# Kernel tuning notes

Measured on AMD Instinct MI355X. Metric: run time of the kernel, lower is better.

The kernel has to match this reference:

```python
import jax, jax.numpy as jnp
import numpy as np

# SLAYER neuron / simulation constants (from params)
THETA = 10.0      # spike threshold
TAU_SR = 10.0     # PSP (synaptic response) time constant
TS = 1.0          # simulation time step
TAU_RHO = 1.0     # surrogate-gradient width
SCALE_RHO = 1.0   # surrogate-gradient scale
ALPHA = float(np.exp(-TS / TAU_SR))  # leaky-filter decay per step

B, C_IN, T = 32, 156, 2048
HID, OUT = 512, 20


@jax.custom_vjp
def spike(u):
    # Hard threshold with SLAYER-style exponential surrogate gradient.
    return (u >= THETA).astype(u.dtype)

def _spike_fwd(u):
    return spike(u), u

def _spike_bwd(u, g):
    sg = (SCALE_RHO / TAU_RHO) * jnp.exp(-jnp.abs(u - THETA) / TAU_RHO)
    return (g * sg,)

spike.defvjp(_spike_fwd, _spike_bwd)


def psp(x):
    # Leaky exponential temporal filter along the LAST axis (SLAYER psp):
    # y[t] = ALPHA * y[t-1] + x[t]
    xt = jnp.moveaxis(x, -1, 0)  # [T, ...]
    def step(c, xi):
        c = ALPHA * c + xi
        return c, c
    _, y = jax.lax.scan(step, jnp.zeros_like(xt[0]), xt)
    return jnp.moveaxis(y, 0, -1)


def dense(x, W):
    # SLAYER dense layer: per-timestep fully-connected over channel dim.
    # x: [N, C, H, W, T], W: [O, C] -> [N, O, H, W, T]
    return jnp.einsum('oc,nchwt->nohwt', W, x)


def _make_perm():
    rng = np.random.default_rng(0)
    random_list = rng.permutation(np.arange(1, 40))
    perm = []
    for i in random_list:
        perm.append(2 * int(i) - 2)
        perm.append(2 * int(i) - 1)
    for i in random_list:
        perm.append(2 * int(i) - 2 + 78)
        perm.append(2 * int(i) - 1 + 78)
    return jnp.asarray(perm, dtype=jnp.int32)


def setup_inputs() -> dict:
    key = jax.random.key(0)
    k0, k1, k2, k3, k4 = jax.random.split(key, 5)
    spike_input = jax.random.randint(k0, (B, C_IN, 1, 1, T), 0, 2).astype(jnp.float32)
    W1 = jax.random.normal(k1, (HID, C_IN), dtype=jnp.float32) * (C_IN ** -0.5)
    W2 = jax.random.normal(k2, (OUT, HID), dtype=jnp.float32) * (HID ** -0.5)
    Wl1 = jax.random.normal(k3, (HID, T), dtype=jnp.float32) * (T ** -0.5)
    Wl2 = jax.random.normal(k4, (OUT, HID), dtype=jnp.float32) * (HID ** -0.5)
    perm = _make_perm()
    return {"spike_input": spike_input, "W1": W1, "W2": W2,
            "Wl1": Wl1, "Wl2": Wl2, "perm": perm}


def reference(spike_input, W1, W2, Wl1, Wl2, perm):
    # Branch 1: channel-dense over taxels, PSP + spike, twice.
    s1 = spike(psp(dense(spike_input, W1)))          # [B, HID, 1, 1, T]
    spike_output = spike(psp(dense(s1, W2)))         # [B, OUT, 1, 1, T]

    # Branch 2: transpose channel<->time, permute taxel axis, dense over time dim.
    x_t = jnp.swapaxes(spike_input, 1, 4)            # [B, T, 1, 1, C_IN]
    x_tp = x_t[..., perm]                            # gather on taxel axis
    l1 = spike(psp(dense(x_tp, Wl1)))                # [B, HID, 1, 1, C_IN]
    location_output = spike(psp(dense(l1, Wl2)))     # [B, OUT, 1, 1, C_IN]

    return jnp.concatenate([spike_output, location_output], axis=4)
```

## Files before the change

kernel.cpp:

```cpp
#include <hip/hip_runtime.h>

#define ALPHA  0.90483741803595952f
#define ALPHA8 0.44932896411722156f
#define THETA  10.0f
#define BF1    ((unsigned short)0x3F80)
#define ISCALE 0.015625f

typedef short   bf16x8 __attribute__((ext_vector_type(8)));
typedef float   f32x4  __attribute__((ext_vector_type(4)));
typedef float   f32x4v __attribute__((ext_vector_type(4)));
typedef unsigned short ushort4v __attribute__((ext_vector_type(4)));
typedef unsigned short ushort8v __attribute__((ext_vector_type(8)));
typedef unsigned char  uchar4v  __attribute__((ext_vector_type(4)));
typedef unsigned char  uchar8v  __attribute__((ext_vector_type(8)));
typedef long long i64;

__device__ __forceinline__ unsigned short f2bf(float f) {
    unsigned int x = __float_as_uint(f);
    unsigned int r = (x + 0x7FFFu + ((x >> 16) & 1u)) >> 16;
    return (unsigned short)r;
}
__device__ __forceinline__ float bf2f(unsigned short h) {
    return __uint_as_float(((unsigned int)h) << 16);
}
__device__ __forceinline__ void split2(float w, unsigned short& h0,
                                       unsigned short& h1) {
    h0 = f2bf(w);          float r0 = w - bf2f(h0);
    h1 = f2bf(r0);
}
__device__ __forceinline__ unsigned char f2fp8(float f) {
    int pk = __builtin_amdgcn_cvt_pk_fp8_f32(f, 0.f, 0, false);
    return (unsigned char)(pk & 0xFF);
}
__device__ __forceinline__ float fp82f(unsigned char b) {
    return __builtin_amdgcn_cvt_f32_fp8((int)b, 0);
}

__global__ __launch_bounds__(256) void prep_scan_pack(
    const float* __restrict__ In, unsigned char* __restrict__ Infp8,
    unsigned short* __restrict__ Pbf,
    const float* __restrict__ W1,  const float* __restrict__ W2,
    const float* __restrict__ Wl1, const float* __restrict__ Wl2,
    unsigned short* __restrict__ W1p,  unsigned char* __restrict__ W2p8,
    unsigned char* __restrict__ Wl1p8, unsigned short* __restrict__ Wl2p)
{
    const int blk = blockIdx.x;
    if (blk >= 4992) {
        const int bidx = blk - 4992;
        if (bidx >= 512 && bidx < 544) {
            int m = bidx - 512;
            for (int k = threadIdx.x; k < 512; k += 256) {
                float w = (m < 20) ? W2[(long long)m * 512 + k] : 0.f;
                unsigned char h0 = f2fp8(w);
                unsigned char h1 = f2fp8(w - fp82f(h0));
                W2p8[(long long)m * 512 + k] = h0;
                W2p8[16384 + (long long)m * 512 + k] = h1;
            }
        } else if (bidx >= 544 && bidx < 1056) {
            int m = bidx - 544;
            for (int k = threadIdx.x; k < 2048; k += 256) {
                float w = Wl1[(long long)m * 2048 + k] * 64.0f;
                unsigned char h0 = f2fp8(w);
                unsigned char h1 = f2fp8(w - fp82f(h0));
                Wl1p8[(long long)m * 2048 + k] = h0;
                Wl1p8[1048576 + (long long)m * 2048 + k] = h1;
            }
        } else {
            const float* W; unsigned short* P; int M, K, Kp, Mp, m;
            if (bidx < 512) { W = W1;  P = W1p;  M = 512; K = 156; Kp = 160; Mp = 512; m = bidx; }
            else            { W = Wl2; P = Wl2p; M = 20;  K = 512; Kp = 512; Mp = 32;  m = bidx - 1056; }
            for (int k = threadIdx.x; k < Kp; k += 256) {
                float v = (m < M && k < K) ? W[(long long)m * K + k] : 0.f;
                unsigned short h0, h1;
                split2(v, h0, h1);
                P[(long long)m * Kp + k] = h0;
                P[(long long)Mp * Kp + (long long)m * Kp + k] = h1;
            }
        }
        return;
    }

    const int row = blk;
    const int tid = threadIdx.x;
    const float* x = In + (long long)row * 2048 + tid * 8;
    const unsigned char ONE8 = f2fp8(1.0f);

    float v[8];
    *(f32x4v*)&v[0] = *(const f32x4v*)x;
    *(f32x4v*)&v[4] = *(const f32x4v*)(x + 4);

    uchar8v raw;
    #pragma unroll
    for (int k = 0; k < 8; ++k) raw[k] = (v[k] >= 0.5f) ? ONE8 : (unsigned char)0;
    *(uchar8v*)(Infp8 + (long long)row * 2048 + tid * 8) = raw;

    float y = 0.f;
    #pragma unroll
    for (int k = 0; k < 8; ++k) { y = ALPHA * y + v[k]; v[k] = y; }

    __shared__ float sc[256];
    float val = y;
    sc[tid] = val;
    float m = ALPHA8;
    for (int d = 1; d < 256; d <<= 1) {
        __syncthreads();
        float p = (tid >= d) ? sc[tid - d] : 0.f;
        __syncthreads();
        val += m * p;
        sc[tid] = val;
        m *= m;
    }
    __syncthreads();
    float carry = (tid > 0) ? sc[tid - 1] : 0.f;

    ushort8v pv;
    float ak = ALPHA;
    #pragma unroll
    for (int k = 0; k < 8; ++k) {
        float yk = v[k] + ak * carry;
        ak *= ALPHA;
        pv[k] = f2bf(yk);
    }
    *(ushort8v*)(Pbf + (long long)row * 2048 + tid * 8) = pv;
}

__global__ __launch_bounds__(256) void transposeP(
    const unsigned short* __restrict__ Pbf, unsigned short* __restrict__ PT)
{
    __shared__ unsigned short Tile[64][72];
    const int t0 = blockIdx.x * 64;
    const int c0 = blockIdx.y * 64;
    const int b  = blockIdx.z;
    const int tid = threadIdx.x;

    #pragma unroll
    for (int s = 0; s < 2; ++s) {
        int id = tid + s * 256;
        int cc = id >> 3;
        int t8 = (id & 7) * 8;
        ushort8v v = {0,0,0,0,0,0,0,0};
        if (c0 + cc < 156)
            v = *(const ushort8v*)(Pbf + (long long)(b * 156 + c0 + cc) * 2048 + t0 + t8);
        *(ushort8v*)&Tile[cc][t8] = v;
    }
    __syncthreads();

    #pragma unroll
    for (int s = 0; s < 2; ++s) {
        int id = tid + s * 256;
        int t  = id >> 3;
        int c8 = (id & 7) * 8;
        if (c0 + c8 + 7 < 160) {
            unsigned short r[8];
            #pragma unroll
            for (int j = 0; j < 8; ++j) r[j] = Tile[c8 + j][t];
            *(ushort8v*)(PT + (long long)b * 327680 + (long long)(t0 + t) * 160 + c0 + c8)
                = *(ushort8v*)r;
        }
    }
}

__global__ __launch_bounds__(256, 4) void mega_gemm1(
    const unsigned short* __restrict__ W1p,
    const unsigned short* __restrict__ PT,
    unsigned short* __restrict__ S1bits,
    const unsigned char* __restrict__ Wl1p8,
    const unsigned char* __restrict__ Infp8,
    unsigned short* __restrict__ Zp)
{
    __shared__ alignas(16) unsigned char SMEM[40960];
    const int bx  = blockIdx.x;
    const int tid = threadIdx.x;
    const int lane = tid & 63, w = tid >> 6;
    const int wy = w >> 1, wx = w & 1;
    const int l15 = lane & 15, kq = lane >> 4;

    if (bx < 4096) {
        auto As = (unsigned short (*)[2][64][40])SMEM;
        auto Bs = (unsigned short (*)[128][40])(SMEM + 20480);

        const int z  = bx >> 7;
        const int m0 = ((bx >> 4) & 7) * 64;
        const int n0 = (bx & 15) * 128;
        const unsigned short* Tb = PT + (long long)z * 327680;

        int aPl[2], aM[2], aK8[2], bT[2], bC8[2];
        #pragma unroll
        for (int s = 0; s < 2; ++s) {
            int id = tid + s * 256;
            aPl[s] = id >> 8; int rem = id & 255;
            aM[s] = rem >> 2; aK8[s] = (rem & 3) * 8;
            bT[s] = id >> 2;  bC8[s] = (id & 3) * 8;
        }

        f32x4 acc[2][4] = {};
        ushort8v aReg[2], bReg[2];

        auto loadAB = [&](int k0) {
            #pragma unroll
            for (int s = 0; s < 2; ++s)
                aReg[s] = *(const ushort8v*)(W1p + (long long)aPl[s] * 81920 +
                                             (long long)(m0 + aM[s]) * 160 + k0 + aK8[s]);
            #pragma unroll
            for (int s = 0; s < 2; ++s)
                bReg[s] = *(const ushort8v*)(Tb + (long long)(n0 + bT[s]) * 160 + k0 + bC8[s]);
        };
        auto stage = [&](int buf) {
            #pragma unroll
            for (int s = 0; s < 2; ++s) *(ushort8v*)&As[buf][aPl[s]][aM[s]][aK8[s]] = aReg[s];
            #pragma unroll
            for (int s = 0; s < 2; ++s) *(ushort8v*)&Bs[buf][bT[s]][bC8[s]] = bReg[s];
        };

        loadAB(0);
        stage(0);
        __syncthreads();

        #pragma unroll
        for (int it = 0; it < 5; ++it) {
            const int cur = it & 1;
            if (it < 4) loadAB((it + 1) * 32);

            bf16x8 bfr[4];
            #pragma unroll
            for (int nt = 0; nt < 4; ++nt)
                bfr[nt] = *(const bf16x8*)&Bs[cur][wx * 64 + nt * 16 + l15][kq * 8];
            #pragma unroll
            for (int s = 0; s < 2; ++s) {
                #pragma unroll
                for (int mt = 0; mt < 2; ++mt) {
                    bf16x8 afr = *(const bf16x8*)&As[cur][s][wy * 32 + mt * 16 + l15][kq * 8];
                    #pragma unroll
                    for (int nt = 0; nt < 4; ++nt)
                        acc[mt][nt] = __builtin_amdgcn_mfma_f32_16x16x32_bf16(
                            afr, bfr[nt], acc[mt][nt], 0, 0, 0);
                }
            }

            if (it < 4) stage(cur ^ 1);
            __syncthreads();
        }

        unsigned short* Db = S1bits + (long long)z * 512 * 128;
        #pragma unroll
        for (int mt = 0; mt < 2; ++mt) {
            #pragma unroll
            for (int i = 0; i < 4; ++i) {
                int m = m0 + wy * 32 + mt * 16 + kq * 4 + i;
                #pragma unroll
                for (int nt = 0; nt < 4; ++nt) {
                    unsigned long long mask = __ballot(acc[mt][nt][i] >= THETA);
                    if (l15 == 0) {
                        int nchunk = (n0 + wx * 64 + nt * 16) >> 4;
                        Db[(long long)m * 128 + nchunk] =
                            (unsigned short)((mask >> (kq * 16)) & 0xFFFFu);
                    }
                }
            }
        }
    } else {
        auto As8 = (unsigned char (*)[2][64][72])SMEM;
        auto Bs8 = (unsigned char (*)[128][72])(SMEM + 18432);

        const int id0 = bx - 4096;
        const int nIdx = id0 % 40;
        if (nIdx >= 39) return;
        const int rest = id0 / 40;
        const int n0  = nIdx * 128;
        const int m0  = (rest & 7) * 64;
        const int ksl = rest >> 3;
        const int ks0 = ksl * 512;

        int aPl[4], aM[4], aK8[4], bN[4], bK8[4];
        #pragma unroll
        for (int s = 0; s < 4; ++s) {
            int id = tid + s * 256;
            aPl[s] = id >> 9; int rem = id & 511;
            aM[s] = rem >> 3; aK8[s] = (rem & 7) * 8;
            bN[s] = id >> 3;  bK8[s] = (id & 7) * 8;
        }

        f32x4 acc[2][4] = {};
        uchar8v aReg[4], bReg[4];

        auto loadAB = [&](int k0) {
            #pragma unroll
            for (int s = 0; s < 4; ++s)
                aReg[s] = *(const uchar8v*)(Wl1p8 + (long long)aPl[s] * 1048576 +
                                            (long long)(m0 + aM[s]) * 2048 + k0 + aK8[s]);
            #pragma unroll
            for (int s = 0; s < 4; ++s)
                bReg[s] = *(const uchar8v*)(Infp8 + (long long)(n0 + bN[s]) * 2048 + k0 + bK8[s]);
        };
        auto stage = [&](int buf) {
            #pragma unroll
            for (int s = 0; s < 4; ++s) *(uchar8v*)&As8[buf][aPl[s]][aM[s]][aK8[s]] = aReg[s];
            #pragma unroll
            for (int s = 0; s < 4; ++s) *(uchar8v*)&Bs8[buf][bN[s]][bK8[s]] = bReg[s];
        };

        loadAB(ks0);
        stage(0);
        __syncthreads();

        for (int it = 0; it < 8; ++it) {
            const int cur = it & 1;
            if (it < 7) loadAB(ks0 + (it + 1) * 64);

            #pragma unroll
            for (int ks = 0; ks < 2; ++ks) {
                i64 bfr[4];
                #pragma unroll
                for (int nt = 0; nt < 4; ++nt)
                    bfr[nt] = *(const i64*)&Bs8[cur][wx * 64 + nt * 16 + l15][ks * 32 + kq * 8];
                #pragma unroll
                for (int s = 0; s < 2; ++s) {
                    #pragma unroll
                    for (int mt = 0; mt < 2; ++mt) {
                        i64 afr = *(const i64*)&As8[cur][s][wy * 32 + mt * 16 + l15][ks * 32 + kq * 8];
                        #pragma unroll
                        for (int nt = 0; nt < 4; ++nt)
                            acc[mt][nt] = __builtin_amdgcn_mfma_f32_16x16x32_fp8_fp8(
                                afr, bfr[nt], acc[mt][nt], 0, 0, 0);
                    }
                }
            }

            if (it < 7) stage(cur ^ 1);
            __syncthreads();
        }

        unsigned short* Tu = (unsigned short*)SMEM;
        #pragma unroll
        for (int mt = 0; mt < 2; ++mt) {
            #pragma unroll
            for (int i = 0; i < 4; ++i) {
                int mL = wy * 32 + mt * 16 + kq * 4 + i;
                #pragma unroll
                for (int nt = 0; nt < 4; ++nt) {
                    int nL = wx * 64 + nt * 16 + l15;
                    Tu[mL * 129 + nL] = f2bf(acc[mt][nt][i] * ISCALE);
                }
            }
        }
        __syncthreads();

        unsigned short* Zs = Zp + (long long)ksl * 2555904;
        #pragma unroll
        for (int s2 = 0; s2 < 32; ++s2) {
            int id = tid + s2 * 256;
            int cL = id >> 6;
            int mL = id & 63;
            int n = n0 + cL;
            int bb = n / 156, cc = n - bb * 156;
            Zs[(long long)cc * 16384 + bb * 512 + m0 + mL] = Tu[mL * 129 + cL];
        }
    }
}

__global__ __launch_bounds__(256) void mega_stage2(
    const unsigned char* __restrict__ W2p8,
    const unsigned short* __restrict__ S1bits,
    float* __restrict__ C2p,
    const unsigned short* __restrict__ Zp,
    const int* __restrict__ perm,
    unsigned short* __restrict__ L1T)
{
    __shared__ alignas(16) unsigned char SMEM[20608];
    const int bx  = blockIdx.x;
    const int tid = threadIdx.x;

    if (bx < 1024) {
        auto As = (unsigned char (*)[32][72])SMEM;
        auto Bs = (unsigned char (*)[72])(SMEM + 4608);

        const int lane = tid & 63, w = tid >> 6;
        const int l15 = lane & 15, kq = lane >> 4;
        const int n0  = (bx & 15) * 128;
        const int ksl = (bx >> 4) & 1;
        const int b   = bx >> 5;
        const int ks0 = ksl * 256;

        const unsigned short* Bb = S1bits + (long long)b * 512 * 128;
        const unsigned char ONE8 = f2fp8(1.0f);

        int aPl[2], aM[2], aK8[2];
        #pragma unroll
        for (int s = 0; s < 2; ++s) {
            int id = tid + s * 256;
            aPl[s] = id >> 8; int rem = id & 255;
            aM[s] = rem >> 3; aK8[s] = (rem & 7) * 8;
        }
        const int kb = (tid >> 4) * 4;
        const int nb = (tid & 15) * 8;
        const int nchunk = (n0 + nb) >> 4;
        const int nshift = nb & 15;

        f32x4 acc[2][2] = {};
        uchar8v aReg[2];
        unsigned short bBits[4];

        auto loadA = [&](int k0) {
            #pragma unroll
            for (int s = 0; s < 2; ++s)
                aReg[s] = *(const uchar8v*)(W2p8 + (long long)aPl[s] * 16384 +
                                            (long long)aM[s] * 512 + k0 + aK8[s]);
        };
        auto loadB = [&](int k0) {
            #pragma unroll
            for (int kk2 = 0; kk2 < 4; ++kk2)
                bBits[kk2] = Bb[(long long)(k0 + kb + kk2) * 128 + nchunk];
        };
        auto stage = [&]() {
            #pragma unroll
            for (int s = 0; s < 2; ++s) *(uchar8v*)&As[aPl[s]][aM[s]][aK8[s]] = aReg[s];
            unsigned char bv[4][8];
            #pragma unroll
            for (int kk2 = 0; kk2 < 4; ++kk2) {
                unsigned int bits = ((unsigned int)bBits[kk2] >> nshift) & 0xFFu;
                #pragma unroll
                for (int j = 0; j < 8; ++j)
                    bv[kk2][j] = ((bits >> j) & 1u) ? ONE8 : (unsigned char)0;
            }
            #pragma unroll
            for (int j = 0; j < 8; ++j) {
                uchar4v v4 = { bv[0][j], bv[1][j], bv[2][j], bv[3][j] };
                *(uchar4v*)&Bs[nb + j][kb] = v4;
            }
        };

        loadA(ks0); loadB(ks0);
        stage();
        __syncthreads();

        #pragma unroll
        for (int it = 0; it < 4; ++it) {
            const int kn = ks0 + (it + 1) * 64;
            if (it < 3) { loadA(kn); loadB(kn); }

            #pragma unroll
            for (int ks = 0; ks < 2; ++ks) {
                i64 bfr[2];
                #pragma unroll
                for (int nt = 0; nt < 2; ++nt)
                    bfr[nt] = *(const i64*)&Bs[w * 32 + nt * 16 + l15][ks * 32 + kq * 8];
                #pragma unroll
                for (int s = 0; s < 2; ++s) {
                    #pragma unroll
                    for (int mt = 0; mt < 2; ++mt) {
                        i64 afr = *(const i64*)&As[s][mt * 16 + l15][ks * 32 + kq * 8];
                        #pragma unroll
                        for (int nt = 0; nt < 2; ++nt)
                            acc[mt][nt] = __builtin_amdgcn_mfma_f32_16x16x32_fp8_fp8(
                                afr, bfr[nt], acc[mt][nt], 0, 0, 0);
                    }
                }
            }
            __syncthreads();
            if (it < 3) {
                stage();
                __syncthreads();
            }
        }

        float* Cb = C2p + (long long)b * 20 * 2048 + (long long)ksl * 1310720LL;
        #pragma unroll
        for (int mt = 0; mt < 2; ++mt) {
            #pragma unroll
            for (int i = 0; i < 4; ++i) {
                int m = mt * 16 + kq * 4 + i;
                if (m >= 20) continue;
                #pragma unroll
                for (int nt = 0; nt < 2; ++nt) {
                    int n = n0 + w * 32 + nt * 16 + l15;
                    Cb[(long long)m * 2048 + n] = acc[mt][nt][i];
                }
            }
        }
    } else {
        auto Xs = (float (*)[32])SMEM;
        int* p  = (int*)(SMEM + 19968);

        const int r0 = (bx - 1024) * 32;
        for (int i = tid; i < 156; i += 256) p[i] = perm[i];

        const int row = tid & 31;
        const int cq  = tid >> 5;
        #pragma unroll
        for (int it = 0; it < 20; ++it) {
            int c = it * 8 + cq;
            if (c < 156) {
                long long base = (long long)c * 16384 + r0 + row;
                float s = bf2f(Zp[base]) + bf2f(Zp[base + 2555904]) +
                          bf2f(Zp[base + 2 * 2555904]) + bf2f(Zp[base + 3 * 2555904]);
                Xs[c][row] = s;
            }
        }
        __syncthreads();

        if (tid < 32) {
            float y = 0.f;
            for (int c = 0; c < 156; ++c) {
                y = ALPHA * y + Xs[p[c]][tid];
                L1T[(long long)c * 16384 + r0 + tid] = (y >= THETA) ? BF1 : 0;
            }
        }
    }
}

__global__ __launch_bounds__(256) void mega_stage3(
    const float* __restrict__ C2p, float* __restrict__ out,
    const unsigned short* __restrict__ Wl2p,
    const unsigned short* __restrict__ L1T)
{
    __shared__ alignas(16) unsigned char SMEM[36864];
    const int bx  = blockIdx.x;
    const int tid = threadIdx.x;

    if (bx < 640) {
        float* sc = (float*)SMEM;
        const int row = bx;
        const float* x = C2p + (long long)row * 2048 + tid * 8;

        float v[8];
        #pragma unroll
        for (int k = 0; k < 8; ++k) v[k] = x[k] + x[k + 1310720LL];

        float y = 0.f;
        #pragma unroll
        for (int k = 0; k < 8; ++k) { y = ALPHA * y + v[k]; v[k] = y; }

        float val = y;
        sc[tid] = val;
        float m = ALPHA8;
        for (int d = 1; d < 256; d <<= 1) {
            __syncthreads();
            float p = (tid >= d) ? sc[tid - d] : 0.f;
            __syncthreads();
            val += m * p;
            sc[tid] = val;
            m *= m;
        }
        __syncthreads();
        float carry = (tid > 0) ? sc[tid - 1] : 0.f;

        float* o = out + (long long)row * 2204 + tid * 8;
        float ak = ALPHA;
        #pragma unroll
        for (int k = 0; k < 8; ++k) {
            float yk = v[k] + ak * carry;
            ak *= ALPHA;
            o[k] = (yk >= THETA) ? 1.0f : 0.0f;
        }
    } else {
        auto As = (unsigned short (*)[32][72])SMEM;
        auto Bs = (unsigned short (*)[72])(SMEM + 9216);

        const int b  = bx - 640;
        const int lane = tid & 63, w = tid >> 6;
        const int l15 = lane & 15, kq = lane >> 4;

        f32x4 acc[2][3] = {};

        for (int k0 = 0; k0 < 512; k0 += 64) {
            #pragma unroll
            for (int s = 0; s < 2; ++s) {
                int id = tid + s * 256;
                int pl = id >> 8, rem = id & 255;
                int m = rem >> 3, k8 = (rem & 7) * 8;
                ushort8v v = *(const ushort8v*)(Wl2p + (long long)pl * 16384 +
                                                (long long)m * 512 + k0 + k8);
                *(ushort8v*)&As[pl][m][k8] = v;
            }
            #pragma unroll
            for (int s = 0; s < 6; ++s) {
                int id = tid + s * 256;
                int n = id >> 3, k8 = (id & 7) * 8;
                ushort8v v = {0,0,0,0,0,0,0,0};
                if (n < 156)
                    v = *(const ushort8v*)(L1T + (long long)n * 16384 +
                                           b * 512 + k0 + k8);
                *(ushort8v*)&Bs[n][k8] = v;
            }
            __syncthreads();

            #pragma unroll
            for (int ks = 0; ks < 2; ++ks) {
                bf16x8 bfr[3];
                #pragma unroll
                for (int nt = 0; nt < 3; ++nt)
                    bfr[nt] = *(const bf16x8*)&Bs[w * 48 + nt * 16 + l15][ks * 32 + kq * 8];
                #pragma unroll
                for (int s = 0; s < 2; ++s) {
                    #pragma unroll
                    for (int mt = 0; mt < 2; ++mt) {
                        bf16x8 afr = *(const bf16x8*)&As[s][mt * 16 + l15][ks * 32 + kq * 8];
                        #pragma unroll
                        for (int nt = 0; nt < 3; ++nt)
                            acc[mt][nt] = __builtin_amdgcn_mfma_f32_16x16x32_bf16(
                                afr, bfr[nt], acc[mt][nt], 0, 0, 0);
                    }
                }
            }
            __syncthreads();
        }

        float* Cs = (float*)SMEM;
        #pragma unroll
        for (int mt = 0; mt < 2; ++mt) {
            #pragma unroll
            for (int i = 0; i < 4; ++i) {
                int m = mt * 16 + kq * 4 + i;
                #pragma unroll
                for (int nt = 0; nt < 3; ++nt) {
                    int n = w * 48 + nt * 16 + l15;
                    Cs[m * 193 + n] = acc[mt][nt][i];
                }
            }
        }
        __syncthreads();

        if (tid < 20) {
            const float* cr = Cs + tid * 193;
            float* o = out + (long long)(b * 20 + tid) * 2204 + 2048;
            float y = 0.f;
            for (int c = 0; c < 156; ++c) {
                y = ALPHA * y + cr[c];
                o[c] = (y >= THETA) ? 1.0f : 0.0f;
            }
        }
    }
}

extern "C" void kernel_launch(void* const* d_in, const int* in_sizes, int n_in,
                              void* d_out, int out_size, void* d_ws, size_t ws_size,
                              hipStream_t stream)
{
    const float* In  = (const float*)d_in[0];
    const float* W1  = (const float*)d_in[1];
    const float* W2  = (const float*)d_in[2];
    const float* Wl1 = (const float*)d_in[3];
    const float* Wl2 = (const float*)d_in[4];
    const int*  perm = (const int*)d_in[5];
    float* out = (float*)d_out;

    float* ws = (float*)d_ws;
    unsigned short* S1bits = (unsigned short*)ws;
    float* C2p = ws + 1048576LL;
    unsigned char*  Infp8 = (unsigned char*)(ws + 3670016LL);
    unsigned short* Pbf  = (unsigned short*)(ws + 6225920LL);
    unsigned short* PT   = (unsigned short*)(ws + 11337728LL);
    unsigned short* W1p  = (unsigned short*)(ws + 16580608LL);
    unsigned char*  W2p8 = (unsigned char*)(ws + 16662528LL);
    unsigned char*  Wl1p8= (unsigned char*)(ws + 16670720LL);
    unsigned short* Wl2p = (unsigned short*)(ws + 17195008LL);
    unsigned short* Zpbf = (unsigned short*)(ws + 17211392LL);
    unsigned short* L1T  = (unsigned short*)(ws + 22323200LL);

    dim3 blk(256);

    prep_scan_pack<<<dim3(6080), blk, 0, stream>>>(
        In, Infp8, Pbf, W1, W2, Wl1, Wl2, W1p, W2p8, Wl1p8, Wl2p);
    transposeP<<<dim3(32, 3, 32), blk, 0, stream>>>(Pbf, PT);

    mega_gemm1<<<dim3(5376), blk, 0, stream>>>(W1p, PT, S1bits,
                                               Wl1p8, Infp8, Zpbf);
    mega_stage2<<<dim3(1536), blk, 0, stream>>>(W2p8, S1bits, C2p,
                                                Zpbf, perm, L1T);
    mega_stage3<<<dim3(672), blk, 0, stream>>>(C2p, out, Wl2p, L1T);

    (void)in_sizes; (void)n_in; (void)out_size; (void)ws_size;
}
```

Baseline: 191.1 us.

## Load GEMM A-operand fragments directly from global into registers, bypassing LDS

In several GEMM kernels the weight (A) tiles are no longer staged through shared memory. Each lane now loads its MFMA fragment straight from global memory into double-buffered registers, and shared memory holds only the B tiles. The block order in mega_gemm1 is also swapped so the fp8 blocks come first. This removes LDS writes, LDS reads and LDS footprint, which can raise occupancy, but it adds redundant global and L2 loads of A across waves and more register pressure.

```diff
diff --git a/kernel.cpp b/kernel.cpp
--- a/kernel.cpp
+++ b/kernel.cpp
@@ -168,68 +168,76 @@
     const unsigned char* __restrict__ Infp8,
     unsigned short* __restrict__ Zp)
 {
-    __shared__ alignas(16) unsigned char SMEM[40960];
+    __shared__ alignas(16) unsigned char SMEM[20480];
     const int bx  = blockIdx.x;
     const int tid = threadIdx.x;
     const int lane = tid & 63, w = tid >> 6;
     const int wy = w >> 1, wx = w & 1;
     const int l15 = lane & 15, kq = lane >> 4;
 
-    if (bx < 4096) {
-        auto As = (unsigned short (*)[2][64][40])SMEM;
-        auto Bs = (unsigned short (*)[128][40])(SMEM + 20480);
-
-        const int z  = bx >> 7;
-        const int m0 = ((bx >> 4) & 7) * 64;
-        const int n0 = (bx & 15) * 128;
+    if (bx >= 1280) {
+        auto Bs = (unsigned short (*)[128][40])SMEM;
+
+        const int id1 = bx - 1280;
+        const int z  = id1 >> 7;
+        const int m0 = ((id1 >> 4) & 7) * 64;
+        const int n0 = (id1 & 15) * 128;
         const unsigned short* Tb = PT + (long long)z * 327680;
 
-        int aPl[2], aM[2], aK8[2], bT[2], bC8[2];
+        int bT[2], bC8[2];
         #pragma unroll
         for (int s = 0; s < 2; ++s) {
             int id = tid + s * 256;
-            aPl[s] = id >> 8; int rem = id & 255;
-            aM[s] = rem >> 2; aK8[s] = (rem & 3) * 8;
             bT[s] = id >> 2;  bC8[s] = (id & 3) * 8;
         }
 
+        const unsigned short* Arow[2][2];
+        #pragma unroll
+        for (int pl = 0; pl < 2; ++pl)
+            #pragma unroll
+            for (int mt = 0; mt < 2; ++mt)
+                Arow[pl][mt] = W1p + (long long)pl * 81920 +
+                               (long long)(m0 + wy * 32 + mt * 16 + l15) * 160 + kq * 8;
+
         f32x4 acc[2][4] = {};
-        ushort8v aReg[2], bReg[2];
-
-        auto loadAB = [&](int k0) {
-            #pragma unroll
-            for (int s = 0; s < 2; ++s)
-                aReg[s] = *(const ushort8v*)(W1p + (long long)aPl[s] * 81920 +
-                                             (long long)(m0 + aM[s]) * 160 + k0 + aK8[s]);
+        ushort8v bReg[2];
+        ushort8v aF[2][4];
+
+        auto loadB = [&](int k0) {
             #pragma unroll
             for (int s = 0; s < 2; ++s)
                 bReg[s] = *(const ushort8v*)(Tb + (long long)(n0 + bT[s]) * 160 + k0 + bC8[s]);
         };
-        auto stage = [&](int buf) {
-            #pragma unroll
-            for (int s = 0; s < 2; ++s) *(ushort8v*)&As[buf][aPl[s]][aM[s]][aK8[s]] = aReg[s];
+        auto stageB = [&](int buf) {
             #pragma unroll
             for (int s = 0; s < 2; ++s) *(ushort8v*)&Bs[buf][bT[s]][bC8[s]] = bReg[s];
         };
-
-        loadAB(0);
-        stage(0);
+        auto loadA = [&](int ph, int k0) {
+            #pragma unroll
+            for (int pl = 0; pl < 2; ++pl)
+                #pragma unroll
+                for (int mt = 0; mt < 2; ++mt)
+                    aF[ph][pl * 2 + mt] = *(const ushort8v*)(Arow[pl][mt] + k0);
+        };
+
+        loadB(0); loadA(0, 0);
+        stageB(0);
         __syncthreads();
 
         #pragma unroll
         for (int it = 0; it < 5; ++it) {
             const int cur = it & 1;
-            if (it < 4) loadAB((it + 1) * 32);
+            if (it < 4) { loadB((it + 1) * 32); loadA(cur ^ 1, (it + 1) * 32); }
 
             bf16x8 bfr[4];
             #pragma unroll
             for (int nt = 0; nt < 4; ++nt)
                 bfr[nt] = *(const bf16x8*)&Bs[cur][wx * 64 + nt * 16 + l15][kq * 8];
             #pragma unroll
-            for (int s = 0; s < 2; ++s) {
+            for (int pl = 0; pl < 2; ++pl) {
                 #pragma unroll
                 for (int mt = 0; mt < 2; ++mt) {
-                    bf16x8 afr = *(const bf16x8*)&As[cur][s][wy * 32 + mt * 16 + l15][kq * 8];
+                    bf16x8 afr = (bf16x8)aF[cur][pl * 2 + mt];
                     #pragma unroll
                     for (int nt = 0; nt < 4; ++nt)
                         acc[mt][nt] = __builtin_amdgcn_mfma_f32_16x16x32_bf16(
@@ -237,8 +245,10 @@
                 }
             }
 
-            if (it < 4) stage(cur ^ 1);
-            __syncthreads();
+            if (it < 4) {
+                stageB(cur ^ 1);
+                __syncthreads();
+            }
         }
 
         unsigned short* Db = S1bits + (long long)z * 512 * 128;
@@ -259,10 +269,9 @@
             }
         }
     } else {
-        auto As8 = (unsigned char (*)[2][64][72])SMEM;
-        auto Bs8 = (unsigned char (*)[128][72])(SMEM + 18432);
-
-        const int id0 = bx - 4096;
+        auto Bs8 = (unsigned char (*)[128][72])SMEM;
+
+        const int id0 = bx;
         const int nIdx = id0 % 40;
         if (nIdx >= 39) return;
         const int rest = id0 / 40;
@@ -271,41 +280,53 @@
         const int ksl = rest >> 3;
         const int ks0 = ksl * 512;
 
-        int aPl[4], aM[4], aK8[4], bN[4], bK8[4];
+        int bN[4], bK8[4];
         #pragma unroll
         for (int s = 0; s < 4; ++s) {
             int id = tid + s * 256;
-            aPl[s] = id >> 9; int rem = id & 511;
-            aM[s] = rem >> 3; aK8[s] = (rem & 7) * 8;
             bN[s] = id >> 3;  bK8[s] = (id & 7) * 8;
         }
 
+        const unsigned char* Arow8[2][2];
+        #pragma unroll
+        for (int pl = 0; pl < 2; ++pl)
+            #pragma unroll
+            for (int mt = 0; mt < 2; ++mt)
+                Arow8[pl][mt] = Wl1p8 + (long long)pl * 1048576 +
+                                (long long)(m0 + wy * 32 + mt * 16 + l15) * 2048 + kq * 8;
+
         f32x4 acc[2][4] = {};
-        uchar8v aReg[4], bReg[4];
-
-        auto loadAB = [&](int k0) {
-            #pragma unroll
-            for (int s = 0; s < 4; ++s)
-                aReg[s] = *(const uchar8v*)(Wl1p8 + (long long)aPl[s] * 1048576 +
-                                            (long long)(m0 + aM[s]) * 2048 + k0 + aK8[s]);
+        uchar8v bReg[4];
+        i64 aF8[2][8];
+
+        auto loadB8 = [&](int k0) {
             #pragma unroll
             for (int s = 0; s < 4; ++s)
                 bReg[s] = *(const uchar8v*)(Infp8 + (long long)(n0 + bN[s]) * 2048 + k0 + bK8[s]);
         };
-        auto stage = [&](int buf) {
-            #pragma unroll
-            for (int s = 0; s < 4; ++s) *(uchar8v*)&As8[buf][aPl[s]][aM[s]][aK8[s]] = aReg[s];
+        auto stageB8 = [&](int buf) {
             #pragma unroll
             for (int s = 0; s < 4; ++s) *(uchar8v*)&Bs8[buf][bN[s]][bK8[s]] = bReg[s];
         };
-
-        loadAB(ks0);
-        stage(0);
-        __syncthreads();
-
+        auto loadA8 = [&](int ph, int k0) {
+            #pragma unroll
+            for (int pl = 0; pl < 2; ++pl)
+                #pragma unroll
+                for (int mt = 0; mt < 2; ++mt)
+                    #pragma unroll
+                    for (int ks = 0; ks < 2; ++ks)
+                        aF8[ph][(pl * 2 + mt) * 2 + ks] =
+                            *(const i64*)(Arow8[pl][mt] + k0 + ks * 32);
+        };
+
+        loadB8(ks0); loadA8(0, ks0);
+        stageB8(0);
+        __syncthreads();
+
+        #pragma unroll
         for (int it = 0; it < 8; ++it) {
             const int cur = it & 1;
-            if (it < 7) loadAB(ks0 + (it + 1) * 64);
+            if (it < 7) { loadB8(ks0 + (it + 1) * 64); loadA8(cur ^ 1, ks0 + (it + 1) * 64); }
 
             #pragma unroll
             for (int ks = 0; ks < 2; ++ks) {
@@ -314,10 +335,10 @@
                 for (int nt = 0; nt < 4; ++nt)
                     bfr[nt] = *(const i64*)&Bs8[cur][wx * 64 + nt * 16 + l15][ks * 32 + kq * 8];
                 #pragma unroll
-                for (int s = 0; s < 2; ++s) {
+                for (int pl = 0; pl < 2; ++pl) {
                     #pragma unroll
                     for (int mt = 0; mt < 2; ++mt) {
-                        i64 afr = *(const i64*)&As8[cur][s][wy * 32 + mt * 16 + l15][ks * 32 + kq * 8];
+                        i64 afr = aF8[cur][(pl * 2 + mt) * 2 + ks];
                         #pragma unroll
                         for (int nt = 0; nt < 4; ++nt)
                             acc[mt][nt] = __builtin_amdgcn_mfma_f32_16x16x32_fp8_fp8(
@@ -326,7 +347,7 @@
                 }
             }
 
-            if (it < 7) stage(cur ^ 1);
+            if (it < 7) stageB8(cur ^ 1);
             __syncthreads();
         }
 
@@ -371,8 +392,7 @@
     const int tid = threadIdx.x;
 
     if (bx < 1024) {
-        auto As = (unsigned char (*)[32][72])SMEM;
-        auto Bs = (unsigned char (*)[72])(SMEM + 4608);
+        auto Bs = (unsigned char (*)[72])SMEM;
 
         const int lane = tid & 63, w = tid >> 6;
         const int l15 = lane & 15, kq = lane >> 4;
@@ -384,27 +404,32 @@
         const unsigned short* Bb = S1bits + (long long)b * 512 * 128;
         const unsigned char ONE8 = f2fp8(1.0f);
 
-        int aPl[2], aM[2], aK8[2];
-        #pragma unroll
-        for (int s = 0; s < 2; ++s) {
-            int id = tid + s * 256;
-            aPl[s] = id >> 8; int rem = id & 255;
-            aM[s] = rem >> 3; aK8[s] = (rem & 7) * 8;
-        }
+        const unsigned char* A2row[2][2];
+        #pragma unroll
+        for (int pl = 0; pl < 2; ++pl)
+            #pragma unroll
+            for (int mt = 0; mt < 2; ++mt)
+                A2row[pl][mt] = W2p8 + (long long)pl * 16384 +
+                                (long long)(mt * 16 + l15) * 512 + kq * 8;
+
         const int kb = (tid >> 4) * 4;
         const int nb = (tid & 15) * 8;
         const int nchunk = (n0 + nb) >> 4;
         const int nshift = nb & 15;
 
         f32x4 acc[2][2] = {};
-        uchar8v aReg[2];
         unsigned short bBits[4];
-
-        auto loadA = [&](int k0) {
-            #pragma unroll
-            for (int s = 0; s < 2; ++s)
-                aReg[s] = *(const uchar8v*)(W2p8 + (long long)aPl[s] * 16384 +
-                                            (long long)aM[s] * 512 + k0 + aK8[s]);
+        i64 aF[2][8];
+
+        auto loadA2 = [&](int ph, int k0) {
+            #pragma unroll
+            for (int pl = 0; pl < 2; ++pl)
+                #pragma unroll
+                for (int mt = 0; mt < 2; ++mt)
+                    #pragma unroll
+                    for (int ks = 0; ks < 2; ++ks)
+                        aF[ph][(pl * 2 + mt) * 2 + ks] =
+                            *(const i64*)(A2row[pl][mt] + k0 + ks * 32);
         };
         auto loadB = [&](int k0) {
             #pragma unroll
@@ -412,8 +437,6 @@
                 bBits[kk2] = Bb[(long long)(k0 + kb + kk2) * 128 + nchunk];
         };
         auto stage = [&]() {
-            #pragma unroll
-            for (int s = 0; s < 2; ++s) *(uchar8v*)&As[aPl[s]][aM[s]][aK8[s]] = aReg[s];
             unsigned char bv[4][8];
             #pragma unroll
             for (int kk2 = 0; kk2 < 4; ++kk2) {
@@ -429,14 +452,15 @@
             }
         };
 
-        loadA(ks0); loadB(ks0);
+        loadB(ks0); loadA2(0, ks0);
         stage();
         __syncthreads();
 
         #pragma unroll
         for (int it = 0; it < 4; ++it) {
+            const int cur = it & 1;
             const int kn = ks0 + (it + 1) * 64;
-            if (it < 3) { loadA(kn); loadB(kn); }
+            if (it < 3) { loadB(kn); loadA2(cur ^ 1, kn); }
 
             #pragma unroll
             for (int ks = 0; ks < 2; ++ks) {
@@ -445,10 +469,10 @@
                 for (int nt = 0; nt < 2; ++nt)
                     bfr[nt] = *(const i64*)&Bs[w * 32 + nt * 16 + l15][ks * 32 + kq * 8];
                 #pragma unroll
-                for (int s = 0; s < 2; ++s) {
+                for (int pl = 0; pl < 2; ++pl) {
                     #pragma unroll
                     for (int mt = 0; mt < 2; ++mt) {
-                        i64 afr = *(const i64*)&As[s][mt * 16 + l15][ks * 32 + kq * 8];
+                        i64 afr = aF[cur][(pl * 2 + mt) * 2 + ks];
                         #pragma unroll
                         for (int nt = 0; nt < 2; ++nt)
                             acc[mt][nt] = __builtin_amdgcn_mfma_f32_16x16x32_fp8_fp8(
@@ -513,7 +537,7 @@
     const unsigned short* __restrict__ Wl2p,
     const unsigned short* __restrict__ L1T)
 {
-    __shared__ alignas(16) unsigned char SMEM[36864];
+    __shared__ alignas(16) unsigned char SMEM[27648];
     const int bx  = blockIdx.x;
     const int tid = threadIdx.x;
 
@@ -553,8 +577,7 @@
             o[k] = (yk >= THETA) ? 1.0f : 0.0f;
         }
     } else {
-        auto As = (unsigned short (*)[32][72])SMEM;
-        auto Bs = (unsigned short (*)[72])(SMEM + 9216);
+        auto Bs = (unsigned short (*)[72])SMEM;
 
         const int b  = bx - 640;
         const int lane = tid & 63, w = tid >> 6;
@@ -563,15 +586,6 @@
         f32x4 acc[2][3] = {};
 
         for (int k0 = 0; k0 < 512; k0 += 64) {
-            #pragma unroll
-            for (int s = 0; s < 2; ++s) {
-                int id = tid + s * 256;
-                int pl = id >> 8, rem = id & 255;
-                int m = rem >> 3, k8 = (rem & 7) * 8;
-                ushort8v v = *(const ushort8v*)(Wl2p + (long long)pl * 16384 +
-                                                (long long)m * 512 + k0 + k8);
-                *(ushort8v*)&As[pl][m][k8] = v;
-            }
             #pragma unroll
             for (int s = 0; s < 6; ++s) {
                 int id = tid + s * 256;
@@ -591,10 +605,12 @@
                 for (int nt = 0; nt < 3; ++nt)
                     bfr[nt] = *(const bf16x8*)&Bs[w * 48 + nt * 16 + l15][ks * 32 + kq * 8];
                 #pragma unroll
-                for (int s = 0; s < 2; ++s) {
+                for (int pl = 0; pl < 2; ++pl) {
                     #pragma unroll
                     for (int mt = 0; mt < 2; ++mt) {
-                        bf16x8 afr = *(const bf16x8*)&As[s][mt * 16 + l15][ks * 32 + kq * 8];
+                        bf16x8 afr = *(const bf16x8*)(Wl2p + (long long)pl * 16384 +
+                                        (long long)(mt * 16 + l15) * 512 +
+                                        k0 + ks * 32 + kq * 8);
                         #pragma unroll
                         for (int nt = 0; nt < 3; ++nt)
                             acc[mt][nt] = __builtin_amdgcn_mfma_f32_16x16x32_bf16(
```

New measurement: 237.7 us. 24.4% more time.

## Use direct global-to-LDS DMA with XOR swizzle and larger GEMM1 tiles

Applied to the files above, without the earlier changes.

Both GEMM paths in mega_gemm1 now stage their operands with global_load_lds 16-byte DMA straight into LDS instead of round-tripping through registers. Bank conflicts are avoided with an XOR swizzle rather than padded rows. The bf16 branch grows its M tile from 64 to 128, giving 4x4 accumulators per wave and fewer blocks. The fp8 branch is reordered to launch first, and launch_bounds no longer requests 4 waves/SIMD, which risks lower occupancy from more registers and a larger LDS footprint.

```diff
diff --git a/kernel.cpp b/kernel.cpp
--- a/kernel.cpp
+++ b/kernel.cpp
@@ -14,6 +14,11 @@
 typedef unsigned char  uchar4v  __attribute__((ext_vector_type(4)));
 typedef unsigned char  uchar8v  __attribute__((ext_vector_type(8)));
 typedef long long i64;
+
+#define DMA16(gsrc, ldst)                                                     \
+    __builtin_amdgcn_global_load_lds(                                         \
+        (const __attribute__((address_space(1))) unsigned int*)(gsrc),        \
+        (__attribute__((address_space(3))) unsigned int*)(ldst), 16, 0, 0)
 
 __device__ __forceinline__ unsigned short f2bf(float f) {
     unsigned int x = __float_as_uint(f);
@@ -160,7 +165,7 @@
     }
 }
 
-__global__ __launch_bounds__(256, 4) void mega_gemm1(
+__global__ __launch_bounds__(256) void mega_gemm1(
     const unsigned short* __restrict__ W1p,
     const unsigned short* __restrict__ PT,
     unsigned short* __restrict__ S1bits,
@@ -168,85 +173,93 @@
     const unsigned char* __restrict__ Infp8,
     unsigned short* __restrict__ Zp)
 {
-    __shared__ alignas(16) unsigned char SMEM[40960];
+    __shared__ alignas(16) unsigned char SMEM[49152];
     const int bx  = blockIdx.x;
     const int tid = threadIdx.x;
     const int lane = tid & 63, w = tid >> 6;
     const int wy = w >> 1, wx = w & 1;
     const int l15 = lane & 15, kq = lane >> 4;
-
-    if (bx < 4096) {
-        auto As = (unsigned short (*)[2][64][40])SMEM;
-        auto Bs = (unsigned short (*)[128][40])(SMEM + 20480);
-
-        const int z  = bx >> 7;
-        const int m0 = ((bx >> 4) & 7) * 64;
-        const int n0 = (bx & 15) * 128;
+    const int key = (l15 >> 1) & 3;
+
+    if (bx >= 1280) {
+        unsigned char* Ab = SMEM;
+        unsigned char* Bb = SMEM + 32768;
+
+        const int id1 = bx - 1280;
+        const int z  = id1 >> 6;
+        const int m0 = ((id1 >> 4) & 3) * 128;
+        const int n0 = (id1 & 15) * 128;
         const unsigned short* Tb = PT + (long long)z * 327680;
 
-        int aPl[2], aM[2], aK8[2], bT[2], bC8[2];
-        #pragma unroll
-        for (int s = 0; s < 2; ++s) {
-            int id = tid + s * 256;
-            aPl[s] = id >> 8; int rem = id & 255;
-            aM[s] = rem >> 2; aK8[s] = (rem & 3) * 8;
-            bT[s] = id >> 2;  bC8[s] = (id & 3) * 8;
-        }
-
-        f32x4 acc[2][4] = {};
-        ushort8v aReg[2], bReg[2];
-
-        auto loadAB = [&](int k0) {
-            #pragma unroll
-            for (int s = 0; s < 2; ++s)
-                aReg[s] = *(const ushort8v*)(W1p + (long long)aPl[s] * 81920 +
-                                             (long long)(m0 + aM[s]) * 160 + k0 + aK8[s]);
-            #pragma unroll
-            for (int s = 0; s < 2; ++s)
-                bReg[s] = *(const ushort8v*)(Tb + (long long)(n0 + bT[s]) * 160 + k0 + bC8[s]);
+        auto dmaA = [&](int buf, int k0) {
+            #pragma unroll
+            for (int s = 0; s < 4; ++s) {
+                int id = tid + s * 256;
+                int pl = id >> 9, m = (id >> 2) & 127, g = id & 3;
+                int gs = g ^ ((m >> 1) & 3);
+                DMA16(W1p + (long long)pl * 81920 +
+                      (long long)(m0 + m) * 160 + k0 + gs * 8,
+                      Ab + buf * 16384 + id * 16);
+            }
         };
-        auto stage = [&](int buf) {
-            #pragma unroll
-            for (int s = 0; s < 2; ++s) *(ushort8v*)&As[buf][aPl[s]][aM[s]][aK8[s]] = aReg[s];
-            #pragma unroll
-            for (int s = 0; s < 2; ++s) *(ushort8v*)&Bs[buf][bT[s]][bC8[s]] = bReg[s];
+        auto dmaB = [&](int buf, int k0) {
+            #pragma unroll
+            for (int s = 0; s < 2; ++s) {
+                int id = tid + s * 256;
+                int n = id >> 2, g = id & 3;
+                int gs = g ^ ((n >> 1) & 3);
+                DMA16(Tb + (long long)(n0 + n) * 160 + k0 + gs * 8,
+                      Bb + buf * 8192 + id * 16);
+            }
         };
 
-        loadAB(0);
-        stage(0);
+        int aOff[2][4], bOff[4];
+        #pragma unroll
+        for (int pl = 0; pl < 2; ++pl)
+            #pragma unroll
+            for (int mt = 0; mt < 4; ++mt)
+                aOff[pl][mt] = pl * 8192 + (wy * 64 + mt * 16 + l15) * 64 +
+                               ((kq ^ key) * 16);
+        #pragma unroll
+        for (int nt = 0; nt < 4; ++nt)
+            bOff[nt] = (wx * 64 + nt * 16 + l15) * 64 + ((kq ^ key) * 16);
+
+        f32x4 acc[4][4] = {};
+
+        dmaA(0, 0); dmaB(0, 0);
         __syncthreads();
 
         #pragma unroll
         for (int it = 0; it < 5; ++it) {
             const int cur = it & 1;
-            if (it < 4) loadAB((it + 1) * 32);
-
+            if (it < 4) { dmaA(cur ^ 1, (it + 1) * 32); dmaB(cur ^ 1, (it + 1) * 32); }
+
+            const unsigned char* Ac = Ab + cur * 16384;
+            const unsigned char* Bc = Bb + cur * 8192;
             bf16x8 bfr[4];
             #pragma unroll
             for (int nt = 0; nt < 4; ++nt)
-                bfr[nt] = *(const bf16x8*)&Bs[cur][wx * 64 + nt * 16 + l15][kq * 8];
-            #pragma unroll
-            for (int s = 0; s < 2; ++s) {
-                #pragma unroll
-                for (int mt = 0; mt < 2; ++mt) {
-                    bf16x8 afr = *(const bf16x8*)&As[cur][s][wy * 32 + mt * 16 + l15][kq * 8];
+                bfr[nt] = *(const bf16x8*)(Bc + bOff[nt]);
+            #pragma unroll
+            for (int pl = 0; pl < 2; ++pl) {
+                #pragma unroll
+                for (int mt = 0; mt < 4; ++mt) {
+                    bf16x8 afr = *(const bf16x8*)(Ac + aOff[pl][mt]);
                     #pragma unroll
                     for (int nt = 0; nt < 4; ++nt)
                         acc[mt][nt] = __builtin_amdgcn_mfma_f32_16x16x32_bf16(
                             afr, bfr[nt], acc[mt][nt], 0, 0, 0);
                 }
             }
-
-            if (it < 4) stage(cur ^ 1);
             __syncthreads();
         }
 
         unsigned short* Db = S1bits + (long long)z * 512 * 128;
         #pragma unroll
-        for (int mt = 0; mt < 2; ++mt) {
+        for (int mt = 0; mt < 4; ++mt) {
             #pragma unroll
             for (int i = 0; i < 4; ++i) {
-                int m = m0 + wy * 32 + mt * 16 + kq * 4 + i;
+                int m = m0 + wy * 64 + mt * 16 + kq * 4 + i;
                 #pragma unroll
                 for (int nt = 0; nt < 4; ++nt) {
                     unsigned long long mask = __ballot(acc[mt][nt][i] >= THETA);
@@ -259,10 +272,10 @@
             }
         }
     } else {
-        auto As8 = (unsigned char (*)[2][64][72])SMEM;
-        auto Bs8 = (unsigned char (*)[128][72])(SMEM + 18432);
-
-        const int id0 = bx - 4096;
+        unsigned char* Ab = SMEM;
+        unsigned char* Bb = SMEM + 16384;
+
+        const int id0 = bx;
         const int nIdx = id0 % 40;
         if (nIdx >= 39) return;
         const int rest = id0 / 40;
@@ -271,53 +284,68 @@
         const int ksl = rest >> 3;
         const int ks0 = ksl * 512;
 
-        int aPl[4], aM[4], aK8[4], bN[4], bK8[4];
-        #pragma unroll
-        for (int s = 0; s < 4; ++s) {
-            int id = tid + s * 256;
-            aPl[s] = id >> 9; int rem = id & 511;
-            aM[s] = rem >> 3; aK8[s] = (rem & 7) * 8;
-            bN[s] = id >> 3;  bK8[s] = (id & 7) * 8;
+        auto dmaA8 = [&](int buf, int kk) {
+            #pragma unroll
+            for (int s = 0; s < 2; ++s) {
+                int id = tid + s * 256;
+                int pl = id >> 8, m = (id >> 2) & 63, g = id & 3;
+                int gs = g ^ ((m >> 1) & 3);
+                DMA16(Wl1p8 + (long long)pl * 1048576 +
+                      (long long)(m0 + m) * 2048 + kk + gs * 16,
+                      Ab + buf * 8192 + id * 16);
+            }
+        };
+        auto dmaB8 = [&](int buf, int kk) {
+            #pragma unroll
+            for (int s = 0; s < 2; ++s) {
+                int id = tid + s * 256;
+                int n = id >> 2, g = id & 3;
+                int gs = g ^ ((n >> 1) & 3);
+                DMA16(Infp8 + (long long)(n0 + n) * 2048 + kk + gs * 16,
+                      Bb + buf * 8192 + id * 16);
+            }
+        };
+
+        int aO8[2][2][2], bO8[4][2];
+        #pragma unroll
+        for (int ks = 0; ks < 2; ++ks) {
+            const int gl = ks * 2 + (kq >> 1);
+            const int sub = ((gl ^ key) * 16) + (kq & 1) * 8;
+            #pragma unroll
+            for (int pl = 0; pl < 2; ++pl)
+                #pragma unroll
+                for (int mt = 0; mt < 2; ++mt)
+                    aO8[pl][mt][ks] = pl * 4096 +
+                        (wy * 32 + mt * 16 + l15) * 64 + sub;
+            #pragma unroll
+            for (int nt = 0; nt < 4; ++nt)
+                bO8[nt][ks] = (wx * 64 + nt * 16 + l15) * 64 + sub;
         }
 
         f32x4 acc[2][4] = {};
-        uchar8v aReg[4], bReg[4];
-
-        auto loadAB = [&](int k0) {
-            #pragma unroll
-            for (int s = 0; s < 4; ++s)
-                aReg[s] = *(const uchar8v*)(Wl1p8 + (long long)aPl[s] * 1048576 +
-                                            (long long)(m0 + aM[s]) * 2048 + k0 + aK8[s]);
-            #pragma unroll
-            for (int s = 0; s < 4; ++s)
-                bReg[s] = *(const uchar8v*)(Infp8 + (long long)(n0 + bN[s]) * 2048 + k0 + bK8[s]);
-        };
-        auto stage = [&](int buf) {
-            #pragma unroll
-            for (int s = 0; s < 4; ++s) *(uchar8v*)&As8[buf][aPl[s]][aM[s]][aK8[s]] = aReg[s];
-            #pragma unroll
-            for (int s = 0; s < 4; ++s) *(uchar8v*)&Bs8[buf][bN[s]][bK8[s]] = bReg[s];
-        };
-
-        loadAB(ks0);
-        stage(0);
-        __syncthreads();
-
+
+        dmaA8(0, ks0); dmaB8(0, ks0);
+        __syncthreads();
+
+        #pragma unroll
         for (int it = 0; it < 8; ++it) {
             const int cur = it & 1;
-            if (it < 7) loadAB(ks0 + (it + 1) * 64);
-
+            if (it < 7) { dmaA8(cur ^ 1, ks0 + (it + 1) * 64);
+                          dmaB8(cur ^ 1, ks0 + (it + 1) * 64); }
+
+            const unsigned char* Ac = Ab + cur * 8192;
+            const unsigned char* Bc = Bb + cur * 8192;
             #pragma unroll
             for (int ks = 0; ks < 2; ++ks) {
                 i64 bfr[4];
                 #pragma unroll
                 for (int nt = 0; nt < 4; ++nt)
-                    bfr[nt] = *(const i64*)&Bs8[cur][wx * 64 + nt * 16 + l15][ks * 32 + kq * 8];
-                #pragma unroll
-                for (int s = 0; s < 2; ++s) {
+                    bfr[nt] = *(const i64*)(Bc + bO8[nt][ks]);
+                #pragma unroll
+                for (int pl = 0; pl < 2; ++pl) {
                     #pragma unroll
                     for (int mt = 0; mt < 2; ++mt) {
-                        i64 afr = *(const i64*)&As8[cur][s][wy * 32 + mt * 16 + l15][ks * 32 + kq * 8];
+                        i64 afr = *(const i64*)(Ac + aO8[pl][mt][ks]);
                         #pragma unroll
                         for (int nt = 0; nt < 4; ++nt)
                             acc[mt][nt] = __builtin_amdgcn_mfma_f32_16x16x32_fp8_fp8(
@@ -325,8 +353,6 @@
                     }
                 }
             }
-
-            if (it < 7) stage(cur ^ 1);
             __syncthreads();
         }
 
@@ -663,7 +689,7 @@
         In, Infp8, Pbf, W1, W2, Wl1, Wl2, W1p, W2p8, Wl1p8, Wl2p);
     transposeP<<<dim3(32, 3, 32), blk, 0, stream>>>(Pbf, PT);
 
-    mega_gemm1<<<dim3(5376), blk, 0, stream>>>(W1p, PT, S1bits,
+    mega_gemm1<<<dim3(3328), blk, 0, stream>>>(W1p, PT, S1bits,
                                                Wl1p8, Infp8, Zpbf);
     mega_stage2<<<dim3(1536), blk, 0, stream>>>(W2p8, S1bits, C2p,
                                                 Zpbf, perm, L1T);
```

Result: faster. 187.0 us (-2.2%).
